# Optimization experiments

Hardware: AMD Instinct MI355X
Metric: run time of the kernel (lower is better)

The kernel has to match this reference:

```python
import jax, jax.numpy as jnp
import numpy as np

HEADS = 4
DIM_HEAD = 32
SCALE = 10.0
DIM = 256


def _l2norm(t):
    # matches torch F.normalize(t, dim=-1): divide by max(||t||_2, eps)
    n = jnp.linalg.norm(t, axis=-1, keepdims=True)
    return t / jnp.maximum(n, 1e-12)


def setup_inputs() -> dict:
    key = jax.random.key(0)
    k1, k2, k3, k4 = jax.random.split(key, 4)
    hidden = HEADS * DIM_HEAD  # 128
    x = jax.random.normal(k1, (4, DIM, 64, 64), jnp.float32)
    # 1x1 conv weights == plain GEMM weights over channel dim
    w_qkv = jax.random.normal(k2, (3 * hidden, DIM), jnp.float32) * (1.0 / np.sqrt(DIM))
    w_out = jax.random.normal(k3, (DIM, hidden), jnp.float32) * (1.0 / np.sqrt(hidden))
    b_out = jax.random.normal(k4, (DIM,), jnp.float32) * 0.01
    return {"x": x, "w_qkv": w_qkv, "w_out": w_out, "b_out": b_out}


def reference(x, w_qkv, w_out, b_out):
    b, c, h, w = x.shape
    n = h * w
    # to_qkv: 1x1 conv, no bias  -> (b, 3*hidden, h, w)
    qkv = jnp.einsum('bchw,oc->bohw', x, w_qkv)
    # chunk(3, dim=1) then rearrange 'b (h c) x y -> b h c (x y)'
    qkv = qkv.reshape(b, 3, HEADS, DIM_HEAD, n)
    q, k, v = qkv[:, 0], qkv[:, 1], qkv[:, 2]  # each (b, heads, d, n)
    # l2norm over last axis (the flattened spatial axis), exactly as in source
    q = _l2norm(q)
    k = _l2norm(k)
    sim = jnp.einsum('bhdi,bhdj->bhij', q, k) * SCALE  # (b, heads, n, n)
    attn = jax.nn.softmax(sim, axis=-1)
    out = jnp.einsum('bhij,bhdj->bhid', attn, v)  # (b, heads, n, d)
    # rearrange 'b h (x y) d -> b (h d) x y'
    out = out.transpose(0, 1, 3, 2).reshape(b, HEADS * DIM_HEAD, h, w)
    # to_out: 1x1 conv with bias
    y = jnp.einsum('bchw,oc->bohw', out, w_out) + b_out[None, :, None, None]
    return y
```

## Files before the change

kernel.cpp:

```cpp
#include <hip/hip_runtime.h>
#include <hip/hip_bf16.h>

typedef unsigned short u16;
typedef unsigned int u32;
typedef __attribute__((ext_vector_type(8))) short bf16x8;
typedef __attribute__((ext_vector_type(4))) float f32x4;

#define MFMA(a, b, c) __builtin_amdgcn_mfma_f32_16x16x32_bf16(a, b, c, 0, 0, 0)

__device__ __forceinline__ u16 f2b(float f) {
    u32 x = __float_as_uint(f);
    return (u16)((x + 0x7fffu + ((x >> 16) & 1u)) >> 16);
}
__device__ __forceinline__ bf16x8 ldb8(const u16* p) {
    return *reinterpret_cast<const bf16x8*>(p);
}
__device__ __forceinline__ int cvt_pk(float lo, float hi) {
    int r;
    asm("v_cvt_pk_bf16_f32 %0, %1, %2" : "=v"(r) : "v"(lo), "v"(hi));
    return r;
}

__global__ void k_convw(const float* wq, const float* wo, u16* wqb, u16* wob) {
    int i4 = (blockIdx.x * 256 + threadIdx.x) * 4;
    const float* s;
    u16* d;
    if (i4 < 384 * 256) { s = wq + i4; d = wqb + i4; }
    else { int j = i4 - 384 * 256; s = wo + j; d = wob + j; }
    float4 v = *(const float4*)s;
    u16 o[4] = {f2b(v.x), f2b(v.y), f2b(v.z), f2b(v.w)};
    *(uint2*)d = *(uint2*)o;
}

__global__ void k_trans(const float* __restrict__ src, u16* __restrict__ dst,
                        const float* __restrict__ scale,
                        int R, int C, int H, long sbB, long shB, int scb, int sch) {
    __shared__ float ld[32][33];
    int p = blockIdx.z;
    int b = p / H, h = p - b * H;
    const float* s = src + (long)b * sbB + (long)h * shB;
    u16* d = dst + (long)p * (long)R * (long)C;
    const float* sc = scale ? (scale + b * scb + h * sch) : nullptr;
    int c0 = blockIdx.x * 32, r0 = blockIdx.y * 32;
    int tx = threadIdx.x, ty = threadIdx.y;
#pragma unroll
    for (int i = 0; i < 4; i++) {
        int r = r0 + ty + 8 * i;
        float f = s[(long)r * C + c0 + tx];
        if (sc) f *= sc[r];
        ld[ty + 8 * i][tx] = f;
    }
    __syncthreads();
#pragma unroll
    for (int i = 0; i < 4; i++) {
        int c = c0 + ty + 8 * i;
        d[(long)c * R + r0 + tx] = f2b(ld[tx][ty + 8 * i]);
    }
}

__global__ __launch_bounds__(256) void k_gemm1(const u16* __restrict__ wqb,
                                               const u16* __restrict__ xt,
                                               float* __restrict__ qkvq,
                                               u16* __restrict__ kt,
                                               u16* __restrict__ vb,
                                               float* __restrict__ sumsq) {
    __shared__ __align__(16) u16 tile[4][64][24];
    int lane = threadIdx.x & 63;
    int wvid = threadIdx.x >> 6;
    int wid = blockIdx.x * 4 + wvid;
    int b = wid / 1536;
    int rem = wid - b * 1536;
    int ot = rem >> 6, ng = rem & 63;
    int o0 = ot * 16, n0 = ng * 64;
    int lr = lane & 15, lg = lane >> 4;
    const u16* A = wqb + (o0 + lr) * 256 + lg * 8;
    const u16* B = xt + ((long)b * 4096 + n0 + lr) * 256 + lg * 8;
    f32x4 z = {0.f, 0.f, 0.f, 0.f};
    f32x4 acc[4] = {z, z, z, z};
#pragma unroll
    for (int kk = 0; kk < 8; kk++) {
        bf16x8 af = ldb8(A + kk * 32);
#pragma unroll
        for (int c = 0; c < 4; c++) {
            bf16x8 bb = ldb8(B + c * 16 * 256 + kk * 32);
            acc[c] = MFMA(af, bb, acc[c]);
        }
    }
    if (o0 < 256) {
        float sr[4];
#pragma unroll
        for (int r = 0; r < 4; r++) {
            sr[r] = acc[0][r] * acc[0][r] + acc[1][r] * acc[1][r]
                  + acc[2][r] * acc[2][r] + acc[3][r] * acc[3][r];
#pragma unroll
            for (int off = 1; off < 16; off <<= 1) sr[r] += __shfl_xor(sr[r], off);
        }
        if (lr == 0) {
#pragma unroll
            for (int r = 0; r < 4; r++)
                atomicAdd(sumsq + b * 256 + o0 + lg * 4 + r, sr[r]);
        }
    }
    if (o0 < 128) {
        float* out = qkvq + (long)b * 524288 + (long)(o0 + lg * 4) * 4096 + n0 + lr;
#pragma unroll
        for (int c = 0; c < 4; c++)
#pragma unroll
            for (int r = 0; r < 4; r++)
                out[r * 4096 + c * 16] = acc[c][r];
    } else if (o0 < 256) {
        int od0 = o0 - 128;
        int h = od0 >> 5;
#pragma unroll
        for (int c = 0; c < 4; c++)
#pragma unroll
            for (int r = 0; r < 4; r++)
                tile[wvid][c * 16 + lr][lg * 4 + r] = f2b(acc[c][r]);
        bf16x8 t0 = *(const bf16x8*)&tile[wvid][lane][0];
        bf16x8 t1 = *(const bf16x8*)&tile[wvid][lane][8];
        u16* dst = kt + ((long)(b * 4 + h)) * 131072 + (long)(n0 + lane) * 32 + (od0 & 16);
        *(bf16x8*)dst = t0;
        *(bf16x8*)(dst + 8) = t1;
    } else {
        u16* out = vb + (long)b * 524288 + (long)(o0 - 256 + lg * 4) * 4096 + n0 + lr;
#pragma unroll
        for (int c = 0; c < 4; c++)
#pragma unroll
            for (int r = 0; r < 4; r++)
                out[r * 4096 + c * 16] = f2b(acc[c][r]);
    }
}

__global__ void k_inv(const float* __restrict__ sumsq, float* __restrict__ inv) {
    int i = blockIdx.x * 256 + threadIdx.x;
    int b = i >> 7, o = i & 127;
    float nq = fmaxf(sqrtf(sumsq[b * 256 + o]), 1e-12f);
    float nk = fmaxf(sqrtf(sumsq[b * 256 + 128 + o]), 1e-12f);
    inv[i] = 14.426950408889634f / (nq * nk);
}

__global__ __launch_bounds__(512, 4) void k_attn(const u16* __restrict__ qt,
                                                 const u16* __restrict__ kt,
                                                 const u16* __restrict__ vb,
                                                 u16* __restrict__ ot) {
    __shared__ __align__(16) u16 ktile[4][2][32][40];
    __shared__ __align__(16) u16 vtile[4][2][32][40];
    __shared__ f32x4 lacc[3][2][2][2][64];
    __shared__ float lls[3][2][2][64];
    int wv = threadIdx.x >> 6, lane = threadIdx.x & 63;
    int isub = wv & 1, js = wv >> 1;
    int t = (isub << 6) | lane;
    int bid = blockIdx.x;
    int swz = (bid & 7) * 128 + (bid >> 3);
    int bh = swz >> 6, iblk = swz & 63;
    int lr = lane & 15, lg = lane >> 4;
    long base = (long)bh * 131072;
    int i0 = iblk * 64 + isub * 32;

    bf16x8 qa[2];
    qa[0] = ldb8(qt + base + (long)(i0 + lr) * 32 + lg * 8);
    qa[1] = ldb8(qt + base + (long)(i0 + 16 + lr) * 32 + lg * 8);

    union { u32 w[4]; bf16x8 v; } ones;
    ones.w[0] = ones.w[1] = ones.w[2] = ones.w[3] = 0x3F803F80u;

    f32x4 z = {0.f, 0.f, 0.f, 0.f};
    f32x4 acc[2][2] = {{z, z}, {z, z}};
    f32x4 accl[2] = {z, z};

    const u16* Kg = kt + base + (long)js * 32768 + t * 8;
    const u16* Vg = vb + base + (long)(t >> 2) * 4096 + js * 1024 + (t & 3) * 8;
    u16* kw0 = &ktile[js][0][t >> 2][(t & 3) * 8];
    u16* vw0 = &vtile[js][0][t >> 2][(t & 3) * 8];
    u16* kw1 = &ktile[js][1][t >> 2][(t & 3) * 8];
    u16* vw1 = &vtile[js][1][t >> 2][(t & 3) * 8];

    {
        uint4 gk = *(const uint4*)Kg;
        uint4 gv = *(const uint4*)Vg;
        *(uint4*)kw0 = gk;
        *(uint4*)vw0 = gv;
    }
    __syncthreads();

    int cur = 0;
    for (int s = 0; s < 32; s++) {
        uint4 gk, gv;
        if (s < 31) {
            gk = *(const uint4*)(Kg + (s + 1) * 1024);
            gv = *(const uint4*)(Vg + (s + 1) * 32);
        }
        const u16* kb_p = &ktile[js][cur][0][0];
        const u16* vb_p = &vtile[js][cur][0][0];
        bf16x8 kb0 = ldb8(kb_p + lr * 40 + lg * 8);
        bf16x8 kb1 = ldb8(kb_p + (16 + lr) * 40 + lg * 8);
        bf16x8 va0 = ldb8(vb_p + lr * 40 + lg * 8);
        bf16x8 va1 = ldb8(vb_p + (16 + lr) * 40 + lg * 8);
#pragma unroll
        for (int tau = 0; tau < 2; tau++) {
            f32x4 s0 = MFMA(kb0, qa[tau], z);
            f32x4 s1 = MFMA(kb1, qa[tau], z);
            float p0[4], p1[4];
#pragma unroll
            for (int r = 0; r < 4; r++) {
                p0[r] = __builtin_amdgcn_exp2f(s0[r]);
                p1[r] = __builtin_amdgcn_exp2f(s1[r]);
            }
            int a0 = cvt_pk(p0[0], p0[1]);
            int a1 = cvt_pk(p0[2], p0[3]);
            int b0 = cvt_pk(p1[0], p1[1]);
            int b1 = cvt_pk(p1[2], p1[3]);
            {
                auto r0_ = __builtin_amdgcn_permlane32_swap(a0, b0, false, false);
                a0 = r0_[0]; b0 = r0_[1];
                auto r1_ = __builtin_amdgcn_permlane32_swap(a1, b1, false, false);
                a1 = r1_[0]; b1 = r1_[1];
                auto r2_ = __builtin_amdgcn_permlane16_swap(a0, b0, false, false);
                a0 = r2_[0]; b0 = r2_[1];
                auto r3_ = __builtin_amdgcn_permlane16_swap(a1, b1, false, false);
                a1 = r3_[0]; b1 = r3_[1];
            }
            union { int w[4]; bf16x8 v; } pu;
            pu.w[0] = a0; pu.w[1] = a1; pu.w[2] = b0; pu.w[3] = b1;
            acc[tau][0] = MFMA(va0, pu.v, acc[tau][0]);
            acc[tau][1] = MFMA(va1, pu.v, acc[tau][1]);
            accl[tau] = MFMA(ones.v, pu.v, accl[tau]);
        }
        if (s < 31) {
            if (cur) { *(uint4*)kw0 = gk; *(uint4*)vw0 = gv; }
            else     { *(uint4*)kw1 = gk; *(uint4*)vw1 = gv; }
        }
        __syncthreads();
        cur ^= 1;
    }

    if (js > 0) {
#pragma unroll
        for (int tau = 0; tau < 2; tau++) {
            lacc[js - 1][isub][tau][0][lane] = acc[tau][0];
            lacc[js - 1][isub][tau][1][lane] = acc[tau][1];
            lls[js - 1][isub][tau][lane] = accl[tau][0];
        }
    }
    __syncthreads();
    if (js == 0) {
        int b = bh >> 2, h = bh & 3;
#pragma unroll
        for (int tau = 0; tau < 2; tau++) {
            float l = accl[tau][0];
#pragma unroll
            for (int jj = 0; jj < 3; jj++) l += lls[jj][isub][tau][lane];
            float linv = 1.0f / l;
            u16* op = ot + ((long)(b * 4096 + i0 + tau * 16 + lr)) * 128 + h * 32;
#pragma unroll
            for (int t2 = 0; t2 < 2; t2++) {
                f32x4 o = acc[tau][t2];
#pragma unroll
                for (int jj = 0; jj < 3; jj++) o += lacc[jj][isub][tau][t2][lane];
#pragma unroll
                for (int s2 = 0; s2 < 2; s2++) {
                    int w = cvt_pk(o[2 * s2] * linv, o[2 * s2 + 1] * linv);
                    *(int*)(op + 16 * t2 + 4 * lg + 2 * s2) = w;
                }
            }
        }
    }
}

__global__ __launch_bounds__(256) void k_gemm2(const u16* __restrict__ wob,
                                               const u16* __restrict__ ot,
                                               const float* __restrict__ bout,
                                               float* __restrict__ y) {
    int lane = threadIdx.x & 63;
    int wid = blockIdx.x * 4 + (threadIdx.x >> 6);
    int b = wid >> 10;
    int rem = wid & 1023;
    int otl = rem >> 6, ng = rem & 63;
    int o0 = otl * 16, n0 = ng * 64;
    int lr = lane & 15, lg = lane >> 4;
    const u16* A = wob + (o0 + lr) * 128 + lg * 8;
    const u16* B = ot + ((long)b * 4096 + n0 + lr) * 128 + lg * 8;
    f32x4 z = {0.f, 0.f, 0.f, 0.f};
    f32x4 acc[4] = {z, z, z, z};
#pragma unroll
    for (int kk = 0; kk < 4; kk++) {
        bf16x8 af = ldb8(A + kk * 32);
#pragma unroll
        for (int c = 0; c < 4; c++) {
            bf16x8 bb = ldb8(B + c * 16 * 128 + kk * 32);
            acc[c] = MFMA(af, bb, acc[c]);
        }
    }
    float bo[4];
#pragma unroll
    for (int r = 0; r < 4; r++) bo[r] = bout[o0 + lg * 4 + r];
    float* out = y + (long)b * 1048576 + (long)(o0 + lg * 4) * 4096 + n0 + lr;
#pragma unroll
    for (int c = 0; c < 4; c++)
#pragma unroll
        for (int r = 0; r < 4; r++)
            out[r * 4096 + c * 16] = acc[c][r] + bo[r];
}

extern "C" void kernel_launch(void* const* d_in, const int* in_sizes, int n_in,
                              void* d_out, int out_size, void* d_ws, size_t ws_size,
                              hipStream_t stream) {
    const float* x    = (const float*)d_in[0];
    const float* wqkv = (const float*)d_in[1];
    const float* wout = (const float*)d_in[2];
    const float* bout = (const float*)d_in[3];
    float* y = (float*)d_out;
    char* ws = (char*)d_ws;

    u16*   wqb   = (u16*)(ws);
    u16*   wob   = (u16*)(ws + 196608);
    u16*   xt    = (u16*)(ws + 262144);
    float* qkvq  = (float*)(ws + 8650752);
    float* inv   = (float*)(ws + 17039360);
    float* sumsq = (float*)(ws + 17041408);
    u16*   qt    = (u16*)(ws + 17045504);
    u16*   kt    = (u16*)(ws + 21239808);
    u16*   vb    = (u16*)(ws + 25434112);
    u16*   ot    = (u16*)(ws + 29628416);

    hipMemsetAsync(sumsq, 0, 4096, stream);
    k_convw<<<128, 256, 0, stream>>>(wqkv, wout, wqb, wob);
    k_trans<<<dim3(128, 8, 4), dim3(32, 8), 0, stream>>>(
        x, xt, nullptr, 256, 4096, 1, 1048576L, 0L, 0, 0);
    k_gemm1<<<1536, 256, 0, stream>>>(wqb, xt, qkvq, kt, vb, sumsq);
    k_inv<<<2, 256, 0, stream>>>(sumsq, inv);
    k_trans<<<dim3(128, 1, 16), dim3(32, 8), 0, stream>>>(
        qkvq, qt, inv, 32, 4096, 4, 524288L, 131072L, 128, 32);
    k_attn<<<1024, 512, 0, stream>>>(qt, kt, vb, ot);
    k_gemm2<<<1024, 256, 0, stream>>>(wob, ot, bout, y);
}
```

Before: 187.9 us.

## Fuse transposes into GEMM1 and attention; stage x in LDS; pre-permute K/V tiles

Removes both k_trans launches. GEMM1 now loads fp32 x directly, converts it to bf16 in shared memory and reuses that tile across 12 output row-tiles per block. The attention kernel scales and transposes Q itself from the fp32 qkv buffer. K/V shared tiles are laid out in MFMA-fragment order, and the tile buffers are unioned with the reduction scratch so occupancy can be raised to 8 waves per SIMD hint. This cuts two kernel launches and the intermediate xt/qt global round-trips, at the cost of LDS bank conflicts from the scalar transposed writes and lower GEMM1 parallelism.

```diff
diff --git a/kernel.cpp b/kernel.cpp
--- a/kernel.cpp
+++ b/kernel.cpp
@@ -32,102 +32,92 @@
     *(uint2*)d = *(uint2*)o;
 }
 
-__global__ void k_trans(const float* __restrict__ src, u16* __restrict__ dst,
-                        const float* __restrict__ scale,
-                        int R, int C, int H, long sbB, long shB, int scb, int sch) {
-    __shared__ float ld[32][33];
-    int p = blockIdx.z;
-    int b = p / H, h = p - b * H;
-    const float* s = src + (long)b * sbB + (long)h * shB;
-    u16* d = dst + (long)p * (long)R * (long)C;
-    const float* sc = scale ? (scale + b * scb + h * sch) : nullptr;
-    int c0 = blockIdx.x * 32, r0 = blockIdx.y * 32;
-    int tx = threadIdx.x, ty = threadIdx.y;
-#pragma unroll
-    for (int i = 0; i < 4; i++) {
-        int r = r0 + ty + 8 * i;
-        float f = s[(long)r * C + c0 + tx];
-        if (sc) f *= sc[r];
-        ld[ty + 8 * i][tx] = f;
-    }
-    __syncthreads();
-#pragma unroll
-    for (int i = 0; i < 4; i++) {
-        int c = c0 + ty + 8 * i;
-        d[(long)c * R + r0 + tx] = f2b(ld[tx][ty + 8 * i]);
-    }
-}
-
 __global__ __launch_bounds__(256) void k_gemm1(const u16* __restrict__ wqb,
-                                               const u16* __restrict__ xt,
+                                               const float* __restrict__ x,
                                                float* __restrict__ qkvq,
                                                u16* __restrict__ kt,
                                                u16* __restrict__ vb,
                                                float* __restrict__ sumsq) {
+    __shared__ __align__(16) u16 xl[64][264];
     __shared__ __align__(16) u16 tile[4][64][24];
-    int lane = threadIdx.x & 63;
-    int wvid = threadIdx.x >> 6;
-    int wid = blockIdx.x * 4 + wvid;
-    int b = wid / 1536;
-    int rem = wid - b * 1536;
-    int ot = rem >> 6, ng = rem & 63;
-    int o0 = ot * 16, n0 = ng * 64;
+    int tid = threadIdx.x;
+    int lane = tid & 63, wvid = tid >> 6;
+    int blk = blockIdx.x;
+    int half = blk & 1, ng = (blk >> 1) & 63, b = blk >> 7;
+    int n0 = ng * 64;
+    {
+        int ci = tid >> 4, nq = (tid & 15) * 4;
+        const float* xb = x + (long)b * 1048576 + n0 + nq;
+#pragma unroll
+        for (int p = 0; p < 16; p++) {
+            int c = ci + p * 16;
+            float4 v = *(const float4*)(xb + (long)c * 4096);
+            xl[nq + 0][c] = f2b(v.x);
+            xl[nq + 1][c] = f2b(v.y);
+            xl[nq + 2][c] = f2b(v.z);
+            xl[nq + 3][c] = f2b(v.w);
+        }
+    }
+    __syncthreads();
     int lr = lane & 15, lg = lane >> 4;
-    const u16* A = wqb + (o0 + lr) * 256 + lg * 8;
-    const u16* B = xt + ((long)b * 4096 + n0 + lr) * 256 + lg * 8;
     f32x4 z = {0.f, 0.f, 0.f, 0.f};
-    f32x4 acc[4] = {z, z, z, z};
-#pragma unroll
-    for (int kk = 0; kk < 8; kk++) {
-        bf16x8 af = ldb8(A + kk * 32);
-#pragma unroll
-        for (int c = 0; c < 4; c++) {
-            bf16x8 bb = ldb8(B + c * 16 * 256 + kk * 32);
-            acc[c] = MFMA(af, bb, acc[c]);
-        }
-    }
-    if (o0 < 256) {
-        float sr[4];
-#pragma unroll
-        for (int r = 0; r < 4; r++) {
-            sr[r] = acc[0][r] * acc[0][r] + acc[1][r] * acc[1][r]
-                  + acc[2][r] * acc[2][r] + acc[3][r] * acc[3][r];
-#pragma unroll
-            for (int off = 1; off < 16; off <<= 1) sr[r] += __shfl_xor(sr[r], off);
-        }
-        if (lr == 0) {
-#pragma unroll
-            for (int r = 0; r < 4; r++)
-                atomicAdd(sumsq + b * 256 + o0 + lg * 4 + r, sr[r]);
-        }
-    }
-    if (o0 < 128) {
-        float* out = qkvq + (long)b * 524288 + (long)(o0 + lg * 4) * 4096 + n0 + lr;
-#pragma unroll
-        for (int c = 0; c < 4; c++)
-#pragma unroll
-            for (int r = 0; r < 4; r++)
-                out[r * 4096 + c * 16] = acc[c][r];
-    } else if (o0 < 256) {
-        int od0 = o0 - 128;
-        int h = od0 >> 5;
-#pragma unroll
-        for (int c = 0; c < 4; c++)
-#pragma unroll
-            for (int r = 0; r < 4; r++)
-                tile[wvid][c * 16 + lr][lg * 4 + r] = f2b(acc[c][r]);
-        bf16x8 t0 = *(const bf16x8*)&tile[wvid][lane][0];
-        bf16x8 t1 = *(const bf16x8*)&tile[wvid][lane][8];
-        u16* dst = kt + ((long)(b * 4 + h)) * 131072 + (long)(n0 + lane) * 32 + (od0 & 16);
-        *(bf16x8*)dst = t0;
-        *(bf16x8*)(dst + 8) = t1;
-    } else {
-        u16* out = vb + (long)b * 524288 + (long)(o0 - 256 + lg * 4) * 4096 + n0 + lr;
-#pragma unroll
-        for (int c = 0; c < 4; c++)
-#pragma unroll
-            for (int r = 0; r < 4; r++)
-                out[r * 4096 + c * 16] = f2b(acc[c][r]);
+#pragma unroll
+    for (int oi = 0; oi < 3; oi++) {
+        int ot = half * 12 + wvid * 3 + oi;
+        int o0 = ot * 16;
+        const u16* A = wqb + (o0 + lr) * 256 + lg * 8;
+        f32x4 acc[4] = {z, z, z, z};
+#pragma unroll
+        for (int kk = 0; kk < 8; kk++) {
+            bf16x8 af = ldb8(A + kk * 32);
+#pragma unroll
+            for (int c4 = 0; c4 < 4; c4++) {
+                bf16x8 bb = ldb8(&xl[c4 * 16 + lr][kk * 32 + lg * 8]);
+                acc[c4] = MFMA(af, bb, acc[c4]);
+            }
+        }
+        if (o0 < 256) {
+            float sr[4];
+#pragma unroll
+            for (int r = 0; r < 4; r++) {
+                sr[r] = acc[0][r] * acc[0][r] + acc[1][r] * acc[1][r]
+                      + acc[2][r] * acc[2][r] + acc[3][r] * acc[3][r];
+#pragma unroll
+                for (int off = 1; off < 16; off <<= 1) sr[r] += __shfl_xor(sr[r], off);
+            }
+            if (lr == 0) {
+#pragma unroll
+                for (int r = 0; r < 4; r++)
+                    atomicAdd(sumsq + b * 256 + o0 + lg * 4 + r, sr[r]);
+            }
+        }
+        if (o0 < 128) {
+            float* out = qkvq + (long)b * 524288 + (long)(o0 + lg * 4) * 4096 + n0 + lr;
+#pragma unroll
+            for (int c4 = 0; c4 < 4; c4++)
+#pragma unroll
+                for (int r = 0; r < 4; r++)
+                    out[r * 4096 + c4 * 16] = acc[c4][r];
+        } else if (o0 < 256) {
+            int od0 = o0 - 128, h = od0 >> 5;
+#pragma unroll
+            for (int c4 = 0; c4 < 4; c4++)
+#pragma unroll
+                for (int r = 0; r < 4; r++)
+                    tile[wvid][c4 * 16 + lr][lg * 4 + r] = f2b(acc[c4][r]);
+            bf16x8 t0 = *(const bf16x8*)&tile[wvid][lane][0];
+            bf16x8 t1 = *(const bf16x8*)&tile[wvid][lane][8];
+            u16* dst = kt + ((long)(b * 4 + h)) * 131072 + (long)(n0 + lane) * 32 + (od0 & 16);
+            *(bf16x8*)dst = t0;
+            *(bf16x8*)(dst + 8) = t1;
+        } else {
+            u16* out = vb + (long)b * 524288 + (long)(o0 - 256 + lg * 4) * 4096 + n0 + lr;
+#pragma unroll
+            for (int c4 = 0; c4 < 4; c4++)
+#pragma unroll
+                for (int r = 0; r < 4; r++)
+                    out[r * 4096 + c4 * 16] = f2b(acc[c4][r]);
+        }
     }
 }
 
@@ -139,14 +129,18 @@
     inv[i] = 14.426950408889634f / (nq * nk);
 }
 
-__global__ __launch_bounds__(512, 4) void k_attn(const u16* __restrict__ qt,
+__global__ __launch_bounds__(512, 8) void k_attn(const float* __restrict__ qkvq,
+                                                 const float* __restrict__ inv,
                                                  const u16* __restrict__ kt,
                                                  const u16* __restrict__ vb,
                                                  u16* __restrict__ ot) {
-    __shared__ __align__(16) u16 ktile[4][2][32][40];
-    __shared__ __align__(16) u16 vtile[4][2][32][40];
-    __shared__ f32x4 lacc[3][2][2][2][64];
-    __shared__ float lls[3][2][2][64];
+    union SmemU {
+        struct { u16 k[4][2][2][64][8]; u16 v[4][2][2][64][8]; } t;
+        struct { f32x4 lacc[3][2][2][2][64]; float lls[3][2][2][64]; } p;
+    };
+    __shared__ __align__(16) SmemU sm;
+    __shared__ __align__(16) u16 qtF[2][2][64][8];
+
     int wv = threadIdx.x >> 6, lane = threadIdx.x & 63;
     int isub = wv & 1, js = wv >> 1;
     int t = (isub << 6) | lane;
@@ -154,34 +148,50 @@
     int swz = (bid & 7) * 128 + (bid >> 3);
     int bh = swz >> 6, iblk = swz & 63;
     int lr = lane & 15, lg = lane >> 4;
+    int b = bh >> 2, head = bh & 3;
     long base = (long)bh * 131072;
-    int i0 = iblk * 64 + isub * 32;
-
-    bf16x8 qa[2];
-    qa[0] = ldb8(qt + base + (long)(i0 + lr) * 32 + lg * 8);
-    qa[1] = ldb8(qt + base + (long)(i0 + 16 + lr) * 32 + lg * 8);
-
-    union { u32 w[4]; bf16x8 v; } ones;
+    int i0g = iblk * 64;
+    int i0 = i0g + isub * 32;
+
+    {
+        int u = threadIdx.x;
+        int d = u >> 4, iq = (u & 15) * 4;
+        const float* qsrc = qkvq + (long)b * 524288 + (long)(head * 32 + d) * 4096 + i0g + iq;
+        float sc = inv[b * 128 + head * 32 + d];
+        float4 v4 = *(const float4*)qsrc;
+        float vv[4] = {v4.x, v4.y, v4.z, v4.w};
+        int lg2 = d >> 3, e = d & 7;
+#pragma unroll
+        for (int q = 0; q < 4; q++) {
+            int i = iq + q;
+            qtF[i >> 5][(i >> 4) & 1][lg2 * 16 + (i & 15)][e] = f2b(vv[q] * sc);
+        }
+    }
+
+    int kperm = (t >> 6) * 512 + (t & 15) * 32 + ((t >> 4) & 3) * 8;
+    int vperm = ((t >> 6) * 16 + (t & 15)) * 4096 + ((t >> 4) & 3) * 8;
+    const u16* Kg = kt + base + js * 32768 + kperm;
+    const u16* Vg = vb + base + js * 1024 + vperm;
+    u16* kws = &sm.t.k[js][0][t >> 6][t & 63][0];
+    u16* vws = &sm.t.v[js][0][t >> 6][t & 63][0];
+
+    union { u32 w[4]; bf16x8 v8; } ones;
     ones.w[0] = ones.w[1] = ones.w[2] = ones.w[3] = 0x3F803F80u;
 
     f32x4 z = {0.f, 0.f, 0.f, 0.f};
     f32x4 acc[2][2] = {{z, z}, {z, z}};
     f32x4 accl[2] = {z, z};
 
-    const u16* Kg = kt + base + (long)js * 32768 + t * 8;
-    const u16* Vg = vb + base + (long)(t >> 2) * 4096 + js * 1024 + (t & 3) * 8;
-    u16* kw0 = &ktile[js][0][t >> 2][(t & 3) * 8];
-    u16* vw0 = &vtile[js][0][t >> 2][(t & 3) * 8];
-    u16* kw1 = &ktile[js][1][t >> 2][(t & 3) * 8];
-    u16* vw1 = &vtile[js][1][t >> 2][(t & 3) * 8];
-
     {
         uint4 gk = *(const uint4*)Kg;
         uint4 gv = *(const uint4*)Vg;
-        *(uint4*)kw0 = gk;
-        *(uint4*)vw0 = gv;
+        *(uint4*)kws = gk;
+        *(uint4*)vws = gv;
     }
     __syncthreads();
+    bf16x8 qa[2];
+    qa[0] = ldb8(&qtF[isub][0][lane][0]);
+    qa[1] = ldb8(&qtF[isub][1][lane][0]);
 
     int cur = 0;
     for (int s = 0; s < 32; s++) {
@@ -190,12 +200,10 @@
             gk = *(const uint4*)(Kg + (s + 1) * 1024);
             gv = *(const uint4*)(Vg + (s + 1) * 32);
         }
-        const u16* kb_p = &ktile[js][cur][0][0];
-        const u16* vb_p = &vtile[js][cur][0][0];
-        bf16x8 kb0 = ldb8(kb_p + lr * 40 + lg * 8);
-        bf16x8 kb1 = ldb8(kb_p + (16 + lr) * 40 + lg * 8);
-        bf16x8 va0 = ldb8(vb_p + lr * 40 + lg * 8);
-        bf16x8 va1 = ldb8(vb_p + (16 + lr) * 40 + lg * 8);
+        bf16x8 kb0 = ldb8(&sm.t.k[js][cur][0][lane][0]);
+        bf16x8 kb1 = ldb8(&sm.t.k[js][cur][1][lane][0]);
+        bf16x8 va0 = ldb8(&sm.t.v[js][cur][0][lane][0]);
+        bf16x8 va1 = ldb8(&sm.t.v[js][cur][1][lane][0]);
 #pragma unroll
         for (int tau = 0; tau < 2; tau++) {
             f32x4 s0 = MFMA(kb0, qa[tau], z);
@@ -224,11 +232,11 @@
             pu.w[0] = a0; pu.w[1] = a1; pu.w[2] = b0; pu.w[3] = b1;
             acc[tau][0] = MFMA(va0, pu.v, acc[tau][0]);
             acc[tau][1] = MFMA(va1, pu.v, acc[tau][1]);
-            accl[tau] = MFMA(ones.v, pu.v, accl[tau]);
+            accl[tau] = MFMA(ones.v8, pu.v, accl[tau]);
         }
         if (s < 31) {
-            if (cur) { *(uint4*)kw0 = gk; *(uint4*)vw0 = gv; }
-            else     { *(uint4*)kw1 = gk; *(uint4*)vw1 = gv; }
+            *(uint4*)(kws + ((cur ^ 1) << 10)) = gk;
+            *(uint4*)(vws + ((cur ^ 1) << 10)) = gv;
         }
         __syncthreads();
         cur ^= 1;
@@ -237,26 +245,25 @@
     if (js > 0) {
 #pragma unroll
         for (int tau = 0; tau < 2; tau++) {
-            lacc[js - 1][isub][tau][0][lane] = acc[tau][0];
-            lacc[js - 1][isub][tau][1][lane] = acc[tau][1];
-            lls[js - 1][isub][tau][lane] = accl[tau][0];
+            sm.p.lacc[js - 1][isub][tau][0][lane] = acc[tau][0];
+            sm.p.lacc[js - 1][isub][tau][1][lane] = acc[tau][1];
+            sm.p.lls[js - 1][isub][tau][lane] = accl[tau][0];
         }
     }
     __syncthreads();
     if (js == 0) {
-        int b = bh >> 2, h = bh & 3;
 #pragma unroll
         for (int tau = 0; tau < 2; tau++) {
             float l = accl[tau][0];
 #pragma unroll
-            for (int jj = 0; jj < 3; jj++) l += lls[jj][isub][tau][lane];
+            for (int jj = 0; jj < 3; jj++) l += sm.p.lls[jj][isub][tau][lane];
             float linv = 1.0f / l;
-            u16* op = ot + ((long)(b * 4096 + i0 + tau * 16 + lr)) * 128 + h * 32;
+            u16* op = ot + ((long)(b * 4096 + i0 + tau * 16 + lr)) * 128 + head * 32;
 #pragma unroll
             for (int t2 = 0; t2 < 2; t2++) {
                 f32x4 o = acc[tau][t2];
 #pragma unroll
-                for (int jj = 0; jj < 3; jj++) o += lacc[jj][isub][tau][t2][lane];
+                for (int jj = 0; jj < 3; jj++) o += sm.p.lacc[jj][isub][tau][t2][lane];
 #pragma unroll
                 for (int s2 = 0; s2 < 2; s2++) {
                     int w = cvt_pk(o[2 * s2] * linv, o[2 * s2 + 1] * linv);
@@ -314,23 +321,17 @@
 
     u16*   wqb   = (u16*)(ws);
     u16*   wob   = (u16*)(ws + 196608);
-    u16*   xt    = (u16*)(ws + 262144);
-    float* qkvq  = (float*)(ws + 8650752);
-    float* inv   = (float*)(ws + 17039360);
-    float* sumsq = (float*)(ws + 17041408);
-    u16*   qt    = (u16*)(ws + 17045504);
-    u16*   kt    = (u16*)(ws + 21239808);
-    u16*   vb    = (u16*)(ws + 25434112);
-    u16*   ot    = (u16*)(ws + 29628416);
+    float* qkvq  = (float*)(ws + 262144);
+    float* inv   = (float*)(ws + 8650752);
+    float* sumsq = (float*)(ws + 8652800);
+    u16*   kt    = (u16*)(ws + 8656896);
+    u16*   vb    = (u16*)(ws + 12851200);
+    u16*   ot    = (u16*)(ws + 17045504);
 
     hipMemsetAsync(sumsq, 0, 4096, stream);
     k_convw<<<128, 256, 0, stream>>>(wqkv, wout, wqb, wob);
-    k_trans<<<dim3(128, 8, 4), dim3(32, 8), 0, stream>>>(
-        x, xt, nullptr, 256, 4096, 1, 1048576L, 0L, 0, 0);
-    k_gemm1<<<1536, 256, 0, stream>>>(wqb, xt, qkvq, kt, vb, sumsq);
+    k_gemm1<<<512, 256, 0, stream>>>(wqb, x, qkvq, kt, vb, sumsq);
     k_inv<<<2, 256, 0, stream>>>(sumsq, inv);
-    k_trans<<<dim3(128, 1, 16), dim3(32, 8), 0, stream>>>(
-        qkvq, qt, inv, 32, 4096, 4, 524288L, 131072L, 128, 32);
-    k_attn<<<1024, 512, 0, stream>>>(qt, kt, vb, ot);
+    k_attn<<<1024, 512, 0, stream>>>(qkvq, inv, kt, vb, ot);
     k_gemm2<<<1024, 256, 0, stream>>>(wob, ot, bout, y);
 }
```

Measured after the change: 169.5 us. 1.11x faster.
